# Optimization experiments

Hardware: AMD Instinct MI355X
Metric: run time of the kernel (lower is better)

Reference implementation:

```python
import jax, jax.numpy as jnp
import numpy as np

R_MAX = 1.0
BASIS_MASK = 0xFF        # low 8 bits -> basis index (basis_size=256)
R_BITS_MASK = 0xFFFF     # next 16 bits -> quantized radius
R_DENOM = 65535.0
INT8_DENOM = 127.0


def setup_inputs() -> dict:
    key = jax.random.key(0)
    k_x, k_c, k_b, k_r, k_s, k_bias = jax.random.split(key, 6)
    B, S, D_in, D_out, BASIS = 4, 2048, 4096, 4096, 256
    x = jax.random.normal(k_x, (B, S, D_in), dtype=jnp.float32)
    codes = jax.random.randint(k_c, (D_out,), 0, 16777216, dtype=jnp.int32)
    basis_table = jax.random.normal(k_b, (BASIS, D_in), dtype=jnp.float32)
    residual_q = jax.random.randint(k_r, (D_out, D_in), 0, 256, dtype=jnp.int32)
    residual_scales = jax.random.uniform(k_s, (D_out,), dtype=jnp.float32) * 0.05
    bias = jax.random.normal(k_bias, (D_out,), dtype=jnp.float32)
    return {"x": x, "codes": codes, "basis_table": basis_table,
            "residual_q": residual_q, "residual_scales": residual_scales,
            "bias": bias}


def decode_weight(codes, basis_table, residual_q, residual_scales):
    # Bitfield decode: low 8 bits = basis index, next 16 bits = quantized radius in [0, r_max].
    idx = codes & BASIS_MASK                                   # [O]
    r = ((codes >> 8) & R_BITS_MASK).astype(jnp.float32) / R_DENOM * R_MAX  # [O]
    base = r[:, None] * basis_table[idx]                       # [O, I]
    resid = (residual_q.astype(jnp.float32) - 128.0) / INT8_DENOM  # dequant int8 residual
    return base + residual_scales[:, None] * resid             # [O, I]


def reference(x, codes, basis_table, residual_q, residual_scales, bias):
    W = decode_weight(codes, basis_table, residual_q, residual_scales)  # [O, I]
    # y = x @ W^T + bias  (fused dequant-matmul in the original CUDA kernel)
    return jnp.einsum("bsi,oi->bso", x, W) + bias
```

## Files before the change

kernel.cpp:

```cpp
#include <hip/hip_runtime.h>


typedef __bf16 bf16x8 __attribute__((ext_vector_type(8)));
typedef float f32x4 __attribute__((ext_vector_type(4)));
typedef int i32x4 __attribute__((ext_vector_type(4)));
typedef unsigned short u16x8 __attribute__((ext_vector_type(8)));

__device__ __forceinline__ unsigned short f2bf(float f) {
    union { float f; unsigned int u; } c; c.f = f;
    unsigned int u = c.u;
    u += 0x7fffu + ((u >> 16) & 1u);
    return (unsigned short)(u >> 16);
}
__device__ __forceinline__ float bf2f(unsigned short h) {
    union { unsigned int u; float f; } c; c.u = ((unsigned int)h) << 16;
    return c.f;
}

__device__ __forceinline__ void load_lds16(const void* g, void* l) {
    __builtin_amdgcn_global_load_lds(
        (__attribute__((address_space(1))) void*)(void*)g,
        (__attribute__((address_space(3))) void*)l,
        16, 0, 0);
}

__device__ __forceinline__ int swz_decode(int p, int row_bytes) {
    const int g = p >> 3, t = p & 7, v = t ^ (g & 7);
    const int row = g * 2 + (v >> 2), chunk = v & 3;
    return row * row_bytes + chunk * 16;
}

__global__ void cvt_bf16_kernel(const float4* __restrict__ in4,
                                ushort4* __restrict__ out4, int n4) {
    int i = blockIdx.x * blockDim.x + threadIdx.x;
    const int stride = gridDim.x * blockDim.x;
    for (; i < n4; i += stride) {
        float4 v = in4[i];
        ushort4 o;
        o.x = f2bf(v.x); o.y = f2bf(v.y); o.z = f2bf(v.z); o.w = f2bf(v.w);
        out4[i] = o;
    }
}

__global__ void quant_x_kernel(const float* __restrict__ x,
                               signed char* __restrict__ xq,
                               float* __restrict__ arow, int K) {
    const int m = blockIdx.x;
    const float* row = x + (size_t)m * K;
    const int base = threadIdx.x * 16;
    float4 v[4];
#pragma unroll
    for (int j = 0; j < 4; ++j) v[j] = *(const float4*)(row + base + j * 4);

    float lmax = 0.f;
#pragma unroll
    for (int j = 0; j < 4; ++j) {
        lmax = fmaxf(lmax, fabsf(v[j].x));
        lmax = fmaxf(lmax, fabsf(v[j].y));
        lmax = fmaxf(lmax, fabsf(v[j].z));
        lmax = fmaxf(lmax, fabsf(v[j].w));
    }
#pragma unroll
    for (int off = 32; off; off >>= 1)
        lmax = fmaxf(lmax, __shfl_xor(lmax, off));
    __shared__ float smax[4];
    if ((threadIdx.x & 63) == 0) smax[threadIdx.x >> 6] = lmax;
    __syncthreads();
    const float mx = fmaxf(fmaxf(smax[0], smax[1]), fmaxf(smax[2], smax[3]));
    const float inv = mx > 0.f ? 127.0f / mx : 0.0f;
    if (threadIdx.x == 0) arow[m] = mx * (1.0f / 127.0f);

    union { signed char c[16]; i32x4 w; } pk;
#pragma unroll
    for (int j = 0; j < 4; ++j) {
        pk.c[j * 4 + 0] = (signed char)(int)rintf(v[j].x * inv);
        pk.c[j * 4 + 1] = (signed char)(int)rintf(v[j].y * inv);
        pk.c[j * 4 + 2] = (signed char)(int)rintf(v[j].z * inv);
        pk.c[j * 4 + 3] = (signed char)(int)rintf(v[j].w * inv);
    }
    *(i32x4*)(xq + (size_t)m * K + base) = pk.w;
}

__global__ void pack_q_kernel(const int4* __restrict__ q4,
                              unsigned int* __restrict__ out, int n4) {
    const int i = blockIdx.x * blockDim.x + threadIdx.x;
    if (i >= n4) return;
    int4 a = q4[i];
    unsigned int w = ((unsigned)(a.x - 128) & 0xFFu)
                   | (((unsigned)(a.y - 128) & 0xFFu) << 8)
                   | (((unsigned)(a.z - 128) & 0xFFu) << 16)
                   | (((unsigned)(a.w - 128) & 0xFFu) << 24);
    out[i] = w;
}

__global__ __launch_bounds__(512) void
p_gemm_kernel(const float* __restrict__ x,
              const unsigned short* __restrict__ Bb,
              unsigned short* __restrict__ Pbf,
              int M, int K) {
    __shared__ __align__(16) float As[2][32 * 64];
    __shared__ __align__(16) unsigned short Bs[2][256 * 64];

    const int tid  = threadIdx.x;
    const int lane = tid & 63;
    const int wv   = tid >> 6;
    const int wr   = wv >> 2;
    const int wc   = wv & 3;
    const int m0 = blockIdx.x * 32;
    const int lr = lane & 15;
    const int kg = lane >> 4;

    f32x4 acc[4];
#pragma unroll
    for (int ni = 0; ni < 4; ++ni) acc[ni] = (f32x4){0.f, 0.f, 0.f, 0.f};

    const int aRow = tid >> 4;
    const int aSrc = (tid & 15) ^ (aRow & 15);
    int bRow[4], bSrc[4];
#pragma unroll
    for (int j = 0; j < 4; ++j) {
        const int p = tid + 512 * j;
        bRow[j] = p >> 3;
        bSrc[j] = (p & 7) ^ (bRow[j] & 7);
    }
    const float* aG = x + (size_t)(m0 + aRow) * K + aSrc * 4;
    const unsigned short* bG[4];
#pragma unroll
    for (int j = 0; j < 4; ++j) bG[j] = Bb + (size_t)bRow[j] * K + bSrc[j] * 8;

#define P_STAGE(bb, k0)                                                        \
    do {                                                                       \
        load_lds16(aG + (k0), (char*)As[bb] + tid * 16);                       \
        _Pragma("unroll") for (int j = 0; j < 4; ++j)                          \
            load_lds16(bG[j] + (k0), (char*)Bs[bb] + (tid + 512 * j) * 16);    \
    } while (0)

    P_STAGE(0, 0);
    const int NT = K >> 6;
    for (int t = 0; t < NT; ++t) {
        const int bb = t & 1;
        if (t + 1 < NT) {
            P_STAGE(bb ^ 1, (t + 1) << 6);
            asm volatile("s_waitcnt vmcnt(5)" ::: "memory");
        } else {
            asm volatile("s_waitcnt vmcnt(0)" ::: "memory");
        }
        __builtin_amdgcn_s_barrier();

        const float* Ab = As[bb];
        const unsigned short* Bbf = Bs[bb];
#pragma unroll
        for (int s = 0; s < 2; ++s) {
            const int r = wr * 16 + lr;
            const int c0 = s * 8 + kg * 2;
            const int ph0 = c0 ^ (r & 15);
            const int ph1 = (c0 + 1) ^ (r & 15);
            f32x4 lo = *(const f32x4*)(Ab + r * 64 + ph0 * 4);
            f32x4 hi = *(const f32x4*)(Ab + r * 64 + ph1 * 4);
            bf16x8 a;
            a[0] = (__bf16)lo[0]; a[1] = (__bf16)lo[1];
            a[2] = (__bf16)lo[2]; a[3] = (__bf16)lo[3];
            a[4] = (__bf16)hi[0]; a[5] = (__bf16)hi[1];
            a[6] = (__bf16)hi[2]; a[7] = (__bf16)hi[3];
#pragma unroll
            for (int ni = 0; ni < 4; ++ni) {
                const int rb = wc * 64 + ni * 16 + lr;
                const int ph = (s * 4 + kg) ^ (rb & 7);
                bf16x8 bfr = __builtin_bit_cast(bf16x8,
                    *(const u16x8*)(Bbf + rb * 64 + ph * 8));
                acc[ni] = __builtin_amdgcn_mfma_f32_16x16x32_bf16(
                    a, bfr, acc[ni], 0, 0, 0);
            }
        }
        __builtin_amdgcn_s_barrier();
    }
#undef P_STAGE

#pragma unroll
    for (int ni = 0; ni < 4; ++ni) {
        const int n = wc * 64 + ni * 16 + lr;
        const int mb = m0 + wr * 16 + kg * 4;
#pragma unroll
        for (int rg = 0; rg < 4; ++rg)
            Pbf[(size_t)(mb + rg) * 256 + n] = f2bf(acc[ni][rg]);
    }
}

__global__ __launch_bounds__(512, 2) void
gemm_i8_kernel(const signed char* __restrict__ Xq,
               const signed char* __restrict__ Qb,
               const float* __restrict__ arow,
               const int* __restrict__ codes,
               const float* __restrict__ scales,
               const float* __restrict__ bias,
               const unsigned short* __restrict__ Pbf,
               float* __restrict__ out,
               int M, int N, int K) {
    __shared__ __align__(16) signed char lds[2 * 65536];

    const int tid  = threadIdx.x;
    const int lane = tid & 63;
    const int wv   = tid >> 6;
    const int wr   = wv >> 2;
    const int wc   = wv & 3;
    const int m0 = blockIdx.x * 256;
    const int n0 = blockIdx.y * 256;
    const int lr = lane & 15;
    const int kg = lane >> 4;
    const int cidx = (((lr & 1) << 2) | kg) ^ ((lr >> 1) & 7);

    const int o0 = swz_decode(tid, 64);
    const int o1 = swz_decode(tid + 512, 64);
    const signed char* aG0 = Xq + (size_t)(m0 + (o0 >> 6)) * K + (o0 & 63);
    const signed char* aG1 = Xq + (size_t)(m0 + (o1 >> 6)) * K + (o1 & 63);
    const signed char* bG0 = Qb + (size_t)(n0 + (o0 >> 6)) * K + (o0 & 63);
    const signed char* bG1 = Qb + (size_t)(n0 + (o1 >> 6)) * K + (o1 & 63);
    const int d0 = tid * 16;
    const int d1 = d0 + 8192;

    i32x4 acc[8][4];
#pragma unroll
    for (int mi = 0; mi < 8; ++mi)
#pragma unroll
        for (int ni = 0; ni < 4; ++ni)
            acc[mi][ni] = (i32x4){0, 0, 0, 0};

    const int raBase = (wr * 64 + (lr >> 1)) * 128 + cidx * 16;
    const int rbBase = 32768 + (wc * 32 + (lr >> 1)) * 128 + cidx * 16;

#define STG_A(bufo, ks, kb)                                                    \
    do {                                                                       \
        load_lds16(aG0 + (kb) + (ks) * 64, lds + (bufo) + (ks) * 16384 + d0);  \
        load_lds16(aG1 + (kb) + (ks) * 64, lds + (bufo) + (ks) * 16384 + d1);  \
    } while (0)
#define STG_B(bufo, ks, kb)                                                    \
    do {                                                                       \
        load_lds16(bG0 + (kb) + (ks) * 64,                                     \
                   lds + (bufo) + 32768 + (ks) * 16384 + d0);                  \
        load_lds16(bG1 + (kb) + (ks) * 64,                                     \
                   lds + (bufo) + 32768 + (ks) * 16384 + d1);                  \
    } while (0)

    STG_A(0, 0, 0); STG_B(0, 0, 0); STG_A(0, 1, 0); STG_B(0, 1, 0);
    asm volatile("s_waitcnt vmcnt(4)" ::: "memory");
    __builtin_amdgcn_s_barrier();

    const int NT = K >> 7;
#pragma unroll 2
    for (int t = 0; t < NT; ++t) {
        const int buf  = (t & 1) << 16;
        const int nbuf = buf ^ 65536;
        const int kb   = (t + 1) << 7;
        const bool pre = (t + 1) < NT;
        i32x4 a[8], b0, b1;

#pragma unroll
        for (int mi = 0; mi < 8; ++mi)
            a[mi] = *(const i32x4*)(lds + buf + raBase + mi * 1024);
        b0 = *(const i32x4*)(lds + buf + rbBase + 0 * 1024);
        b1 = *(const i32x4*)(lds + buf + rbBase + 1 * 1024);
        if (pre) STG_A(nbuf, 0, kb);
        __builtin_amdgcn_s_barrier();
        asm volatile("s_waitcnt lgkmcnt(0)" ::: "memory");
        __builtin_amdgcn_s_setprio(1);
#pragma unroll
        for (int mi = 0; mi < 8; ++mi)
            acc[mi][0] = __builtin_amdgcn_mfma_i32_16x16x64_i8(a[mi], b0,
                                                               acc[mi][0], 0, 0, 0);
#pragma unroll
        for (int mi = 0; mi < 8; ++mi)
            acc[mi][1] = __builtin_amdgcn_mfma_i32_16x16x64_i8(a[mi], b1,
                                                               acc[mi][1], 0, 0, 0);
        __builtin_amdgcn_s_setprio(0);
        __builtin_amdgcn_s_barrier();

        b0 = *(const i32x4*)(lds + buf + rbBase + 2 * 1024);
        b1 = *(const i32x4*)(lds + buf + rbBase + 3 * 1024);
        if (pre) STG_B(nbuf, 0, kb);
        __builtin_amdgcn_s_barrier();
        asm volatile("s_waitcnt lgkmcnt(0)" ::: "memory");
        __builtin_amdgcn_s_setprio(1);
#pragma unroll
        for (int mi = 0; mi < 8; ++mi)
            acc[mi][2] = __builtin_amdgcn_mfma_i32_16x16x64_i8(a[mi], b0,
                                                               acc[mi][2], 0, 0, 0);
#pragma unroll
        for (int mi = 0; mi < 8; ++mi)
            acc[mi][3] = __builtin_amdgcn_mfma_i32_16x16x64_i8(a[mi], b1,
                                                               acc[mi][3], 0, 0, 0);
        __builtin_amdgcn_s_setprio(0);
        if (pre) asm volatile("s_waitcnt vmcnt(4)" ::: "memory");
        else     asm volatile("s_waitcnt vmcnt(0)" ::: "memory");
        __builtin_amdgcn_s_barrier();

#pragma unroll
        for (int mi = 0; mi < 8; ++mi)
            a[mi] = *(const i32x4*)(lds + buf + 16384 + raBase + mi * 1024);
        b0 = *(const i32x4*)(lds + buf + 16384 + rbBase + 0 * 1024);
        b1 = *(const i32x4*)(lds + buf + 16384 + rbBase + 1 * 1024);
        if (pre) STG_A(nbuf, 1, kb);
        __builtin_amdgcn_s_barrier();
        asm volatile("s_waitcnt lgkmcnt(0)" ::: "memory");
        __builtin_amdgcn_s_setprio(1);
#pragma unroll
        for (int mi = 0; mi < 8; ++mi)
            acc[mi][0] = __builtin_amdgcn_mfma_i32_16x16x64_i8(a[mi], b0,
                                                               acc[mi][0], 0, 0, 0);
#pragma unroll
        for (int mi = 0; mi < 8; ++mi)
            acc[mi][1] = __builtin_amdgcn_mfma_i32_16x16x64_i8(a[mi], b1,
                                                               acc[mi][1], 0, 0, 0);
        __builtin_amdgcn_s_setprio(0);
        __builtin_amdgcn_s_barrier();

        b0 = *(const i32x4*)(lds + buf + 16384 + rbBase + 2 * 1024);
        b1 = *(const i32x4*)(lds + buf + 16384 + rbBase + 3 * 1024);
        if (pre) STG_B(nbuf, 1, kb);
        __builtin_amdgcn_s_barrier();
        asm volatile("s_waitcnt lgkmcnt(0)" ::: "memory");
        __builtin_amdgcn_s_setprio(1);
#pragma unroll
        for (int mi = 0; mi < 8; ++mi)
            acc[mi][2] = __builtin_amdgcn_mfma_i32_16x16x64_i8(a[mi], b0,
                                                               acc[mi][2], 0, 0, 0);
#pragma unroll
        for (int mi = 0; mi < 8; ++mi)
            acc[mi][3] = __builtin_amdgcn_mfma_i32_16x16x64_i8(a[mi], b1,
                                                               acc[mi][3], 0, 0, 0);
        __builtin_amdgcn_s_setprio(0);
        if (pre) asm volatile("s_waitcnt vmcnt(4)" ::: "memory");
        __builtin_amdgcn_s_barrier();
    }
#undef STG_A
#undef STG_B

    const int mwb = m0 + wr * 128 + kg * 4;
    float av[8][4];
#pragma unroll
    for (int mi = 0; mi < 8; ++mi)
#pragma unroll
        for (int rg = 0; rg < 4; ++rg)
            av[mi][rg] = arow[mwb + mi * 16 + rg];

#pragma unroll
    for (int ni = 0; ni < 4; ++ni) {
        const int n = n0 + wc * 64 + ni * 16 + lr;
        const int code = codes[n];
        const int cc = code & 0xFF;
        const float rr = (float)((code >> 8) & 0xFFFF) * (1.0f / 65535.0f);
        const float so = scales[n] * (1.0f / 127.0f);
        const float bv = bias[n];
#pragma unroll
        for (int mi = 0; mi < 8; ++mi) {
            const int mbase = mwb + mi * 16;
            unsigned short pv[4];
#pragma unroll
            for (int rg = 0; rg < 4; ++rg)
                pv[rg] = Pbf[(size_t)(mbase + rg) * 256 + cc];
#pragma unroll
            for (int rg = 0; rg < 4; ++rg) {
                const float y = av[mi][rg] * so * (float)acc[mi][ni][rg]
                              + rr * bf2f(pv[rg]) + bv;
                __builtin_nontemporal_store(y, &out[(size_t)(mbase + rg) * N + n]);
            }
        }
    }
}

extern "C" void kernel_launch(void* const* d_in, const int* in_sizes, int n_in,
                              void* d_out, int out_size, void* d_ws, size_t ws_size,
                              hipStream_t stream) {
    const float* x        = (const float*)d_in[0];
    const int*   codes    = (const int*)d_in[1];
    const float* basis    = (const float*)d_in[2];
    const int*   q        = (const int*)d_in[3];
    const float* scales   = (const float*)d_in[4];
    const float* bias     = (const float*)d_in[5];
    float* out = (float*)d_out;

    const int BASIS = 256;
    const int K = in_sizes[2] / BASIS;
    const int N = in_sizes[1];
    const int M = in_sizes[0] / K;

    char* ws = (char*)d_ws;
    signed char* Xq = (signed char*)ws;
    size_t off = (size_t)M * K;
    signed char* Qb = (signed char*)(ws + off);
    off += (size_t)N * K;
    unsigned short* Pbf = (unsigned short*)(ws + off);
    off += (size_t)M * 256 * 2;
    float* Arow = (float*)(ws + off);
    off += (size_t)M * sizeof(float);
    unsigned short* Bb = (unsigned short*)(ws + off);

    cvt_bf16_kernel<<<1024, 256, 0, stream>>>((const float4*)basis, (ushort4*)Bb,
                                              BASIS * K / 4);
    p_gemm_kernel<<<M / 32, 512, 0, stream>>>(x, Bb, Pbf, M, K);
    quant_x_kernel<<<M, 256, 0, stream>>>(x, Xq, Arow, K);
    pack_q_kernel<<<(N * K / 4 + 255) / 256, 256, 0, stream>>>(
        (const int4*)q, (unsigned int*)Qb, N * K / 4);
    gemm_i8_kernel<<<dim3(M / 256, N / 256), 512, 0, stream>>>(
        Xq, Qb, Arow, codes, scales, bias, Pbf, out, M, N, K);
}
```

Measured before the change: 522.5 us.

## Deepen int8 GEMM LDS prefetch pipeline and split fragments into 4x4 halves

Restructures the main K loop so global-to-LDS prefetches run up to two tiles ahead instead of one. Stages are reissued into the current buffer as soon as it is consumed, with vmcnt(10) waits and clamped tail indices replacing the conditional prefetch. The MFMA sub-steps now load 4 A and 4 B fragments and issue 4x4 MFMAs each, instead of 8 A by 2 B, which changes register pressure and LDS read counts. The tail clamps to NT-1 and redundantly reloads the last tile, adding some wasted loads. The correctness of buffer reuse depends on the barrier placement.

```diff
diff --git a/kernel.cpp b/kernel.cpp
--- a/kernel.cpp
+++ b/kernel.cpp
@@ -241,98 +241,98 @@
                    lds + (bufo) + 32768 + (ks) * 16384 + d1);                  \
     } while (0)
 
-    STG_A(0, 0, 0); STG_B(0, 0, 0); STG_A(0, 1, 0); STG_B(0, 1, 0);
-    asm volatile("s_waitcnt vmcnt(4)" ::: "memory");
+    const int NT = K >> 7;
+
+    STG_B(0, 0, 0);       STG_A(0, 0, 0);
+    STG_B(0, 1, 0);       STG_A(0, 1, 0);
+    STG_B(65536, 0, 128); STG_A(65536, 0, 128);
+    STG_B(65536, 1, 128);
+    asm volatile("s_waitcnt vmcnt(10)" ::: "memory");
     __builtin_amdgcn_s_barrier();
 
-    const int NT = K >> 7;
 #pragma unroll 2
     for (int t = 0; t < NT; ++t) {
         const int buf  = (t & 1) << 16;
         const int nbuf = buf ^ 65536;
-        const int kb   = (t + 1) << 7;
-        const bool pre = (t + 1) < NT;
-        i32x4 a[8], b0, b1;
-
-#pragma unroll
-        for (int mi = 0; mi < 8; ++mi)
+        const int kb1 = ((t + 1 < NT) ? t + 1 : NT - 1) << 7;
+        const int kb2 = ((t + 2 < NT) ? t + 2 : NT - 1) << 7;
+        i32x4 a[4], b[4];
+
+#pragma unroll
+        for (int mi = 0; mi < 4; ++mi)
             a[mi] = *(const i32x4*)(lds + buf + raBase + mi * 1024);
-        b0 = *(const i32x4*)(lds + buf + rbBase + 0 * 1024);
-        b1 = *(const i32x4*)(lds + buf + rbBase + 1 * 1024);
-        if (pre) STG_A(nbuf, 0, kb);
+#pragma unroll
+        for (int ni = 0; ni < 4; ++ni)
+            b[ni] = *(const i32x4*)(lds + buf + rbBase + ni * 1024);
+        STG_A(nbuf, 1, kb1);
         __builtin_amdgcn_s_barrier();
         asm volatile("s_waitcnt lgkmcnt(0)" ::: "memory");
         __builtin_amdgcn_s_setprio(1);
 #pragma unroll
-        for (int mi = 0; mi < 8; ++mi)
-            acc[mi][0] = __builtin_amdgcn_mfma_i32_16x16x64_i8(a[mi], b0,
-                                                               acc[mi][0], 0, 0, 0);
-#pragma unroll
-        for (int mi = 0; mi < 8; ++mi)
-            acc[mi][1] = __builtin_amdgcn_mfma_i32_16x16x64_i8(a[mi], b1,
-                                                               acc[mi][1], 0, 0, 0);
+        for (int ni = 0; ni < 4; ++ni)
+#pragma unroll
+            for (int mi = 0; mi < 4; ++mi)
+                acc[mi][ni] = __builtin_amdgcn_mfma_i32_16x16x64_i8(
+                    a[mi], b[ni], acc[mi][ni], 0, 0, 0);
         __builtin_amdgcn_s_setprio(0);
         __builtin_amdgcn_s_barrier();
 
-        b0 = *(const i32x4*)(lds + buf + rbBase + 2 * 1024);
-        b1 = *(const i32x4*)(lds + buf + rbBase + 3 * 1024);
-        if (pre) STG_B(nbuf, 0, kb);
+#pragma unroll
+        for (int mi = 0; mi < 4; ++mi)
+            a[mi] = *(const i32x4*)(lds + buf + raBase + (mi + 4) * 1024);
+        STG_B(buf, 0, kb2);
         __builtin_amdgcn_s_barrier();
         asm volatile("s_waitcnt lgkmcnt(0)" ::: "memory");
         __builtin_amdgcn_s_setprio(1);
 #pragma unroll
-        for (int mi = 0; mi < 8; ++mi)
-            acc[mi][2] = __builtin_amdgcn_mfma_i32_16x16x64_i8(a[mi], b0,
-                                                               acc[mi][2], 0, 0, 0);
-#pragma unroll
-        for (int mi = 0; mi < 8; ++mi)
-            acc[mi][3] = __builtin_amdgcn_mfma_i32_16x16x64_i8(a[mi], b1,
-                                                               acc[mi][3], 0, 0, 0);
+        for (int ni = 0; ni < 4; ++ni)
+#pragma unroll
+            for (int mi = 0; mi < 4; ++mi)
+                acc[mi + 4][ni] = __builtin_amdgcn_mfma_i32_16x16x64_i8(
+                    a[mi], b[ni], acc[mi + 4][ni], 0, 0, 0);
         __builtin_amdgcn_s_setprio(0);
-        if (pre) asm volatile("s_waitcnt vmcnt(4)" ::: "memory");
-        else     asm volatile("s_waitcnt vmcnt(0)" ::: "memory");
-        __builtin_amdgcn_s_barrier();
-
-#pragma unroll
-        for (int mi = 0; mi < 8; ++mi)
+        asm volatile("s_waitcnt vmcnt(10)" ::: "memory");
+        __builtin_amdgcn_s_barrier();
+
+#pragma unroll
+        for (int mi = 0; mi < 4; ++mi)
             a[mi] = *(const i32x4*)(lds + buf + 16384 + raBase + mi * 1024);
-        b0 = *(const i32x4*)(lds + buf + 16384 + rbBase + 0 * 1024);
-        b1 = *(const i32x4*)(lds + buf + 16384 + rbBase + 1 * 1024);
-        if (pre) STG_A(nbuf, 1, kb);
+#pragma unroll
+        for (int ni = 0; ni < 4; ++ni)
+            b[ni] = *(const i32x4*)(lds + buf + 16384 + rbBase + ni * 1024);
+        STG_A(buf, 0, kb2);
         __builtin_amdgcn_s_barrier();
         asm volatile("s_waitcnt lgkmcnt(0)" ::: "memory");
         __builtin_amdgcn_s_setprio(1);
 #pragma unroll
-        for (int mi = 0; mi < 8; ++mi)
-            acc[mi][0] = __builtin_amdgcn_mfma_i32_16x16x64_i8(a[mi], b0,
-                                                               acc[mi][0], 0, 0, 0);
-#pragma unroll
-        for (int mi = 0; mi < 8; ++mi)
-            acc[mi][1] = __builtin_amdgcn_mfma_i32_16x16x64_i8(a[mi], b1,
-                                                               acc[mi][1], 0, 0, 0);
+        for (int ni = 0; ni < 4; ++ni)
+#pragma unroll
+            for (int mi = 0; mi < 4; ++mi)
+                acc[mi][ni] = __builtin_amdgcn_mfma_i32_16x16x64_i8(
+                    a[mi], b[ni], acc[mi][ni], 0, 0, 0);
         __builtin_amdgcn_s_setprio(0);
         __builtin_amdgcn_s_barrier();
 
-        b0 = *(const i32x4*)(lds + buf + 16384 + rbBase + 2 * 1024);
-        b1 = *(const i32x4*)(lds + buf + 16384 + rbBase + 3 * 1024);
-        if (pre) STG_B(nbuf, 1, kb);
+#pragma unroll
+        for (int mi = 0; mi < 4; ++mi)
+            a[mi] = *(const i32x4*)(lds + buf + 16384 + raBase + (mi + 4) * 1024);
+        STG_B(buf, 1, kb2);
         __builtin_amdgcn_s_barrier();
         asm volatile("s_waitcnt lgkmcnt(0)" ::: "memory");
         __builtin_amdgcn_s_setprio(1);
 #pragma unroll
-        for (int mi = 0; mi < 8; ++mi)
-            acc[mi][2] = __builtin_amdgcn_mfma_i32_16x16x64_i8(a[mi], b0,
-                                                               acc[mi][2], 0, 0, 0);
-#pragma unroll
-        for (int mi = 0; mi < 8; ++mi)
-            acc[mi][3] = __builtin_amdgcn_mfma_i32_16x16x64_i8(a[mi], b1,
-                                                               acc[mi][3], 0, 0, 0);
+        for (int ni = 0; ni < 4; ++ni)
+#pragma unroll
+            for (int mi = 0; mi < 4; ++mi)
+                acc[mi + 4][ni] = __builtin_amdgcn_mfma_i32_16x16x64_i8(
+                    a[mi], b[ni], acc[mi + 4][ni], 0, 0, 0);
         __builtin_amdgcn_s_setprio(0);
-        if (pre) asm volatile("s_waitcnt vmcnt(4)" ::: "memory");
+        asm volatile("s_waitcnt vmcnt(10)" ::: "memory");
         __builtin_amdgcn_s_barrier();
     }
 #undef STG_A
 #undef STG_B
+    asm volatile("s_waitcnt vmcnt(0)" ::: "memory");
 
     const int mwb = m0 + wr * 128 + kg * 4;
     float av[8][4];
```

Result: faster. 511.6 us (-2.1%).
